# Optimization experiments

Measured on AMD Instinct MI355X. Metric: run time of the kernel, lower is better.

## Reference

```python
import jax, jax.numpy as jnp
import numpy as np

D_MODEL = 1024
NUM_EXPERTS = 64
TOP_K = 2
TEMPERATURE = 1.0


def setup_inputs() -> dict:
    key = jax.random.key(0)
    k1, k2, k3, k4 = jax.random.split(key, 4)
    mh_output = jax.random.normal(k1, (8, 4096, D_MODEL), dtype=jnp.float32)
    noise = jax.random.normal(k2, (8, 4096, NUM_EXPERTS), dtype=jnp.float32)  # randn_like sample, externalized
    # nn.Linear weights: shape [out, in], init normal(0, 0.02); biases zero
    W_route = jax.random.normal(k3, (NUM_EXPERTS, D_MODEL), dtype=jnp.float32) * 0.02
    b_route = jnp.zeros((NUM_EXPERTS,), dtype=jnp.float32)
    W_noise = jax.random.normal(k4, (NUM_EXPERTS, D_MODEL), dtype=jnp.float32) * 0.02
    b_noise = jnp.zeros((NUM_EXPERTS,), dtype=jnp.float32)
    return {"mh_output": mh_output, "noise": noise, "W_route": W_route,
            "b_route": b_route, "W_noise": W_noise, "b_noise": b_noise}


def reference(mh_output, noise, W_route, b_route, W_noise, b_noise):
    # logits = topkroute_linear(mh_output); noise_logits = noise_linear(mh_output)
    logits = jnp.einsum('bsd,ed->bse', mh_output, W_route) + b_route
    noise_logits = jnp.einsum('bsd,ed->bse', mh_output, W_noise) + b_noise
    # noisy logits = logits + temperature * randn * softplus(noise_logits)
    noisy = logits + TEMPERATURE * noise * jax.nn.softplus(noise_logits)
    # top-k, scatter into -inf, softmax  ==  softmax over top-k values scattered into zeros
    top_vals, indices = jax.lax.top_k(noisy, TOP_K)          # [b, s, k]
    probs_k = jax.nn.softmax(top_vals, axis=-1)              # softmax(-inf elsewhere) -> 0 elsewhere
    one_hot = jax.nn.one_hot(indices, NUM_EXPERTS, dtype=noisy.dtype)  # [b, s, k, E]
    router_output = jnp.sum(one_hot * probs_k[..., None], axis=-2)     # [b, s, E]
    return router_output, indices
```

## Files before the change

kernel.cpp:

```cpp
#include <hip/hip_runtime.h>
#include <hip/hip_bf16.h>
#include <math.h>


#define T_TOKENS 32768
#define D_MODEL  1024
#define NE       64
#define NCOL     128
#define M_TILE   32
#define NCHUNK   32
#define CS_LD    68
#define OUT_IDX_BASE ((size_t)T_TOKENS * NE)
#define W_ELEMS  (NCOL * D_MODEL)

typedef short  bf16x8  __attribute__((ext_vector_type(8)));
typedef float  floatx4 __attribute__((ext_vector_type(4)));

__device__ __forceinline__ float softplus_f(float x) {
    return fmaxf(x, 0.f) + log1pf(expf(-fabsf(x)));
}

__device__ __forceinline__ void cvt8(const float4 a, const float4 b,
                                     int4* hi, int4* lo) {
    float v[8] = {a.x, a.y, a.z, a.w, b.x, b.y, b.z, b.w};
    int hw[4], lw[4];
    #pragma unroll
    for (int p = 0; p < 4; ++p) {
        float2 f2 = make_float2(v[2 * p], v[2 * p + 1]);
        __hip_bfloat162 h2 = __float22bfloat162_rn(f2);
        int u; __builtin_memcpy(&u, &h2, 4);
        float h0 = __uint_as_float(((unsigned)u) << 16);
        float h1 = __uint_as_float(((unsigned)u) & 0xFFFF0000u);
        float2 l2 = make_float2(v[2 * p] - h0, v[2 * p + 1] - h1);
        __hip_bfloat162 L2 = __float22bfloat162_rn(l2);
        int ul; __builtin_memcpy(&ul, &L2, 4);
        hw[p] = u; lw[p] = ul;
    }
    *hi = make_int4(hw[0], hw[1], hw[2], hw[3]);
    *lo = make_int4(lw[0], lw[1], lw[2], lw[3]);
}

__device__ __forceinline__ void cvt8r(const float4 a, const float4 b,
                                      bf16x8* hi, bf16x8* lo) {
    int4 h, l;
    cvt8(a, b, &h, &l);
    __builtin_memcpy(hi, &h, 16);
    __builtin_memcpy(lo, &l, 16);
}

__global__ __launch_bounds__(256) void prepack_w(
    const float* __restrict__ Wr, const float* __restrict__ Wn,
    short* __restrict__ Bh, short* __restrict__ Bl)
{
    int g   = blockIdx.x * 256 + threadIdx.x;
    int n   = g & 15;
    int kg  = (g >> 4) & 127;
    int t2  = g >> 11;
    int col = t2 * 16 + n;
    const float* src = (col < NE ? Wr + (size_t)col * D_MODEL
                                 : Wn + (size_t)(col - NE) * D_MODEL) + kg * 8;
    float4 a = *(const float4*)src;
    float4 b = *(const float4*)(src + 4);
    int4 hi, lo;
    cvt8(a, b, &hi, &lo);
    *(int4*)(Bh + (size_t)g * 8) = hi;
    *(int4*)(Bl + (size_t)g * 8) = lo;
}

__global__ __launch_bounds__(256, 4) void router_mfma(
    const float* __restrict__ A,
    const float* __restrict__ noise,
    const float* __restrict__ br,
    const float* __restrict__ bn,
    const short* __restrict__ Bh,
    const short* __restrict__ Bl,
    float* __restrict__ out)
{
    __shared__ float Cs[M_TILE * CS_LD];
    __shared__ float s_p1[M_TILE], s_p2[M_TILE];
    __shared__ int   s_e1[M_TILE], s_e2[M_TILE];

    const int tid  = threadIdx.x;
    const int lane = tid & 63;
    const int wid  = tid >> 6;
    const int n16  = lane & 15;
    const int quad = lane >> 4;
    const int m0   = blockIdx.x * M_TILE;

    const float* pA0 = A + (size_t)(m0 + n16) * D_MODEL + quad * 8;
    const float* pA1 = pA0 + (size_t)16 * D_MODEL;

    const short* pBhR = Bh + ((size_t)(wid * 128 + quad) * 16 + n16) * 8;
    const short* pBlR = Bl + ((size_t)(wid * 128 + quad) * 16 + n16) * 8;
    const short* pBhN = Bh + ((size_t)((4 + wid) * 128 + quad) * 16 + n16) * 8;
    const short* pBlN = Bl + ((size_t)((4 + wid) * 128 + quad) * 16 + n16) * 8;

    floatx4 acc[2][2];
    #pragma unroll
    for (int i = 0; i < 2; ++i) { acc[i][0] = (floatx4)0.f; acc[i][1] = (floatx4)0.f; }

    float4 c0a = *(const float4*)(pA0);
    float4 c0b = *(const float4*)(pA0 + 4);
    float4 c1a = *(const float4*)(pA1);
    float4 c1b = *(const float4*)(pA1 + 4);
    float4 n0a = *(const float4*)(pA0 + 32);
    float4 n0b = *(const float4*)(pA0 + 36);
    float4 n1a = *(const float4*)(pA1 + 32);
    float4 n1b = *(const float4*)(pA1 + 36);

    for (int kc = 0; kc < NCHUNK; ++kc) {
        float4 t0a, t0b, t1a, t1b;
        if (kc + 2 < NCHUNK) {
            const float* q0 = pA0 + (kc + 2) * 32;
            const float* q1 = pA1 + (kc + 2) * 32;
            t0a = *(const float4*)(q0);
            t0b = *(const float4*)(q0 + 4);
            t1a = *(const float4*)(q1);
            t1b = *(const float4*)(q1 + 4);
        }

        const int o = kc * 512;
        bf16x8 bhR = *(const bf16x8*)(pBhR + o);
        bf16x8 blR = *(const bf16x8*)(pBlR + o);
        bf16x8 bhN = *(const bf16x8*)(pBhN + o);
        bf16x8 blN = *(const bf16x8*)(pBlN + o);

        bf16x8 ah0, al0, ah1, al1;
        cvt8r(c0a, c0b, &ah0, &al0);
        cvt8r(c1a, c1b, &ah1, &al1);

        acc[0][0] = __builtin_amdgcn_mfma_f32_16x16x32_bf16(ah0, bhR, acc[0][0], 0, 0, 0);
        acc[0][0] = __builtin_amdgcn_mfma_f32_16x16x32_bf16(ah0, blR, acc[0][0], 0, 0, 0);
        acc[0][0] = __builtin_amdgcn_mfma_f32_16x16x32_bf16(al0, bhR, acc[0][0], 0, 0, 0);
        acc[0][1] = __builtin_amdgcn_mfma_f32_16x16x32_bf16(ah0, bhN, acc[0][1], 0, 0, 0);
        acc[0][1] = __builtin_amdgcn_mfma_f32_16x16x32_bf16(ah0, blN, acc[0][1], 0, 0, 0);
        acc[0][1] = __builtin_amdgcn_mfma_f32_16x16x32_bf16(al0, bhN, acc[0][1], 0, 0, 0);
        acc[1][0] = __builtin_amdgcn_mfma_f32_16x16x32_bf16(ah1, bhR, acc[1][0], 0, 0, 0);
        acc[1][0] = __builtin_amdgcn_mfma_f32_16x16x32_bf16(ah1, blR, acc[1][0], 0, 0, 0);
        acc[1][0] = __builtin_amdgcn_mfma_f32_16x16x32_bf16(al1, bhR, acc[1][0], 0, 0, 0);
        acc[1][1] = __builtin_amdgcn_mfma_f32_16x16x32_bf16(ah1, bhN, acc[1][1], 0, 0, 0);
        acc[1][1] = __builtin_amdgcn_mfma_f32_16x16x32_bf16(ah1, blN, acc[1][1], 0, 0, 0);
        acc[1][1] = __builtin_amdgcn_mfma_f32_16x16x32_bf16(al1, bhN, acc[1][1], 0, 0, 0);

        c0a = n0a; c0b = n0b; c1a = n1a; c1b = n1b;
        n0a = t0a; n0b = t0b; n1a = t1a; n1b = t1b;
    }

    {
        int e = wid * 16 + n16;
        float brv = br[e], bnv = bn[e];
        #pragma unroll
        for (int mf = 0; mf < 2; ++mf)
            #pragma unroll
            for (int rr = 0; rr < 4; ++rr) {
                int t = mf * 16 + quad * 4 + rr;
                float nz    = noise[(size_t)(m0 + t) * NE + e];
                float route = acc[mf][0][rr] + brv;
                float nl    = acc[mf][1][rr] + bnv;
                Cs[t * CS_LD + e] = fmaf(nz, softplus_f(nl), route);
            }
    }
    __syncthreads();

    if (tid < M_TILE) {
        const int t = tid;
        float v1 = -INFINITY, v2 = -INFINITY;
        int e1 = 0, e2 = 0;
        #pragma unroll
        for (int e4 = 0; e4 < 16; ++e4) {
            float4 q = *(const float4*)&Cs[t * CS_LD + e4 * 4];
            float qa[4] = {q.x, q.y, q.z, q.w};
            #pragma unroll
            for (int c = 0; c < 4; ++c) {
                float v = qa[c];
                int e = e4 * 4 + c;
                if (v > v1) { v2 = v1; e2 = e1; v1 = v; e1 = e; }
                else if (v > v2) { v2 = v; e2 = e; }
            }
        }
        float ex = expf(v2 - v1);
        float denom = 1.f + ex;
        s_p1[t] = 1.f / denom;
        s_p2[t] = ex / denom;
        s_e1[t] = e1;
        s_e2[t] = e2;
        float2 iv = make_float2((float)e1, (float)e2);
        *(float2*)(out + OUT_IDX_BASE + (size_t)(m0 + t) * 2) = iv;
    }
    __syncthreads();

    #pragma unroll
    for (int i = 0; i < 2; ++i) {
        int gi = i * 256 + tid;
        int t  = gi >> 4;
        int e0 = (gi & 15) * 4;
        float p1 = s_p1[t], p2 = s_p2[t];
        int   e1 = s_e1[t], e2 = s_e2[t];
        float4 v;
        v.x = (e0 + 0 == e1) ? p1 : ((e0 + 0 == e2) ? p2 : 0.f);
        v.y = (e0 + 1 == e1) ? p1 : ((e0 + 1 == e2) ? p2 : 0.f);
        v.z = (e0 + 2 == e1) ? p1 : ((e0 + 2 == e2) ? p2 : 0.f);
        v.w = (e0 + 3 == e1) ? p1 : ((e0 + 3 == e2) ? p2 : 0.f);
        *(float4*)(out + (size_t)(m0 + t) * NE + e0) = v;
    }
}

extern "C" void kernel_launch(void* const* d_in, const int* in_sizes, int n_in,
                              void* d_out, int out_size, void* d_ws, size_t ws_size,
                              hipStream_t stream) {
    const float* A     = (const float*)d_in[0];
    const float* noise = (const float*)d_in[1];
    const float* Wr    = (const float*)d_in[2];
    const float* br    = (const float*)d_in[3];
    const float* Wn    = (const float*)d_in[4];
    const float* bn    = (const float*)d_in[5];
    float* out = (float*)d_out;

    short* Bh = (short*)d_ws;
    short* Bl = Bh + W_ELEMS;

    prepack_w<<<dim3(W_ELEMS / 8 / 256), dim3(256), 0, stream>>>(Wr, Wn, Bh, Bl);
    router_mfma<<<dim3(T_TOKENS / M_TILE), dim3(256), 0, stream>>>(A, noise, br, bn, Bh, Bl, out);
}
```

Baseline: 261.3 us.

## Stream activation tiles via global_load_lds ring buffer with doubled token tile

Replaces per-thread register prefetch of the fp32 activations with asynchronous global-to-LDS loads into a 4-deep swizzled ring buffer, synchronized with explicit vmcnt waits and barriers. The token tile doubles from 32 to 64, so each weight fragment load is reused across four MFMA row groups, and weight fragments are now prefetched one chunk ahead. The aim is to hide memory latency and halve weight traffic per token. In exchange, occupancy drops from 4 to 2 blocks per SM, LDS use rises, and every chunk now needs a block-wide barrier.

Measured after the change: 236.8 us. 1.1x faster.

```diff
diff --git a/kernel.cpp b/kernel.cpp
--- a/kernel.cpp
+++ b/kernel.cpp
@@ -7,14 +7,17 @@
 #define D_MODEL  1024
 #define NE       64
 #define NCOL     128
-#define M_TILE   32
+#define M_TILE   64
 #define NCHUNK   32
+#define RING_D   4
 #define CS_LD    68
 #define OUT_IDX_BASE ((size_t)T_TOKENS * NE)
 #define W_ELEMS  (NCOL * D_MODEL)
 
 typedef short  bf16x8  __attribute__((ext_vector_type(8)));
 typedef float  floatx4 __attribute__((ext_vector_type(4)));
+typedef const __attribute__((address_space(1))) unsigned int gu32;
+typedef __attribute__((address_space(3))) unsigned int lu32;
 
 __device__ __forceinline__ float softplus_f(float x) {
     return fmaxf(x, 0.f) + log1pf(expf(-fabsf(x)));
@@ -67,7 +70,7 @@
     *(int4*)(Bl + (size_t)g * 8) = lo;
 }
 
-__global__ __launch_bounds__(256, 4) void router_mfma(
+__global__ __launch_bounds__(256, 2) void router_mfma(
     const float* __restrict__ A,
     const float* __restrict__ noise,
     const float* __restrict__ br,
@@ -76,6 +79,7 @@
     const short* __restrict__ Bl,
     float* __restrict__ out)
 {
+    __shared__ __align__(16) float ringA[RING_D * M_TILE * 32];
     __shared__ float Cs[M_TILE * CS_LD];
     __shared__ float s_p1[M_TILE], s_p2[M_TILE];
     __shared__ int   s_e1[M_TILE], s_e2[M_TILE];
@@ -87,70 +91,89 @@
     const int quad = lane >> 4;
     const int m0   = blockIdx.x * M_TILE;
 
-    const float* pA0 = A + (size_t)(m0 + n16) * D_MODEL + quad * 8;
-    const float* pA1 = pA0 + (size_t)16 * D_MODEL;
+    const int rlo = lane >> 3;
+    const int csw = ((lane & 7) ^ rlo) * 4;
+    const int j0  = 2 * wid;
+    const float* srcA0 = A + (size_t)(m0 + j0 * 8 + rlo) * D_MODEL + csw;
+    const float* srcA1 = A + (size_t)(m0 + j0 * 8 + 8 + rlo) * D_MODEL + csw;
+
+    const int sw0 = (((quad * 32 +  0) ^ ((n16 & 7) << 4)) >> 2);
+    const int sw1 = (((quad * 32 + 16) ^ ((n16 & 7) << 4)) >> 2);
 
     const short* pBhR = Bh + ((size_t)(wid * 128 + quad) * 16 + n16) * 8;
     const short* pBlR = Bl + ((size_t)(wid * 128 + quad) * 16 + n16) * 8;
     const short* pBhN = Bh + ((size_t)((4 + wid) * 128 + quad) * 16 + n16) * 8;
     const short* pBlN = Bl + ((size_t)((4 + wid) * 128 + quad) * 16 + n16) * 8;
 
-    floatx4 acc[2][2];
+#define DMA_CHUNK(KC_) do {                                                   \
+        const int b_ = (KC_) & (RING_D - 1);                                  \
+        __builtin_amdgcn_global_load_lds(                                     \
+            (gu32*)(srcA0 + (KC_) * 32),                                      \
+            (lu32*)(ringA + b_ * (M_TILE * 32) + j0 * 256), 16, 0, 0);        \
+        __builtin_amdgcn_global_load_lds(                                     \
+            (gu32*)(srcA1 + (KC_) * 32),                                      \
+            (lu32*)(ringA + b_ * (M_TILE * 32) + (j0 + 1) * 256), 16, 0, 0);  \
+    } while (0)
+
+    floatx4 acc[4][2];
     #pragma unroll
-    for (int i = 0; i < 2; ++i) { acc[i][0] = (floatx4)0.f; acc[i][1] = (floatx4)0.f; }
-
-    float4 c0a = *(const float4*)(pA0);
-    float4 c0b = *(const float4*)(pA0 + 4);
-    float4 c1a = *(const float4*)(pA1);
-    float4 c1b = *(const float4*)(pA1 + 4);
-    float4 n0a = *(const float4*)(pA0 + 32);
-    float4 n0b = *(const float4*)(pA0 + 36);
-    float4 n1a = *(const float4*)(pA1 + 32);
-    float4 n1b = *(const float4*)(pA1 + 36);
+    for (int i = 0; i < 4; ++i) { acc[i][0] = (floatx4)0.f; acc[i][1] = (floatx4)0.f; }
+
+    DMA_CHUNK(0);
+    DMA_CHUNK(1);
+    DMA_CHUNK(2);
+    bf16x8 bhR = *(const bf16x8*)(pBhR);
+    bf16x8 blR = *(const bf16x8*)(pBlR);
+    bf16x8 bhN = *(const bf16x8*)(pBhN);
+    bf16x8 blN = *(const bf16x8*)(pBlN);
 
     for (int kc = 0; kc < NCHUNK; ++kc) {
-        float4 t0a, t0b, t1a, t1b;
-        if (kc + 2 < NCHUNK) {
-            const float* q0 = pA0 + (kc + 2) * 32;
-            const float* q1 = pA1 + (kc + 2) * 32;
-            t0a = *(const float4*)(q0);
-            t0b = *(const float4*)(q0 + 4);
-            t1a = *(const float4*)(q1);
-            t1b = *(const float4*)(q1 + 4);
+        const int buf = kc & (RING_D - 1);
+
+        __builtin_amdgcn_sched_barrier(0);
+        if (kc < NCHUNK - 2)       asm volatile("s_waitcnt vmcnt(4)" ::: "memory");
+        else if (kc == NCHUNK - 2) asm volatile("s_waitcnt vmcnt(2)" ::: "memory");
+        else                       asm volatile("s_waitcnt vmcnt(0)" ::: "memory");
+        __builtin_amdgcn_s_barrier();
+        __builtin_amdgcn_sched_barrier(0);
+
+        if (kc + RING_D - 1 < NCHUNK) DMA_CHUNK(kc + RING_D - 1);
+
+        const int on = (kc + 1 < NCHUNK ? kc + 1 : kc) * 512;
+        bf16x8 nbhR = *(const bf16x8*)(pBhR + on);
+        bf16x8 nblR = *(const bf16x8*)(pBlR + on);
+        bf16x8 nbhN = *(const bf16x8*)(pBhN + on);
+        bf16x8 nblN = *(const bf16x8*)(pBlN + on);
+
+        float4 fa[4], fb[4];
+        #pragma unroll
+        for (int mf = 0; mf < 4; ++mf) {
+            const float* p = &ringA[buf * (M_TILE * 32) + (mf * 16 + n16) * 32];
+            fa[mf] = *(const float4*)(p + sw0);
+            fb[mf] = *(const float4*)(p + sw1);
         }
 
-        const int o = kc * 512;
-        bf16x8 bhR = *(const bf16x8*)(pBhR + o);
-        bf16x8 blR = *(const bf16x8*)(pBlR + o);
-        bf16x8 bhN = *(const bf16x8*)(pBhN + o);
-        bf16x8 blN = *(const bf16x8*)(pBlN + o);
-
-        bf16x8 ah0, al0, ah1, al1;
-        cvt8r(c0a, c0b, &ah0, &al0);
-        cvt8r(c1a, c1b, &ah1, &al1);
-
-        acc[0][0] = __builtin_amdgcn_mfma_f32_16x16x32_bf16(ah0, bhR, acc[0][0], 0, 0, 0);
-        acc[0][0] = __builtin_amdgcn_mfma_f32_16x16x32_bf16(ah0, blR, acc[0][0], 0, 0, 0);
-        acc[0][0] = __builtin_amdgcn_mfma_f32_16x16x32_bf16(al0, bhR, acc[0][0], 0, 0, 0);
-        acc[0][1] = __builtin_amdgcn_mfma_f32_16x16x32_bf16(ah0, bhN, acc[0][1], 0, 0, 0);
-        acc[0][1] = __builtin_amdgcn_mfma_f32_16x16x32_bf16(ah0, blN, acc[0][1], 0, 0, 0);
-        acc[0][1] = __builtin_amdgcn_mfma_f32_16x16x32_bf16(al0, bhN, acc[0][1], 0, 0, 0);
-        acc[1][0] = __builtin_amdgcn_mfma_f32_16x16x32_bf16(ah1, bhR, acc[1][0], 0, 0, 0);
-        acc[1][0] = __builtin_amdgcn_mfma_f32_16x16x32_bf16(ah1, blR, acc[1][0], 0, 0, 0);
-        acc[1][0] = __builtin_amdgcn_mfma_f32_16x16x32_bf16(al1, bhR, acc[1][0], 0, 0, 0);
-        acc[1][1] = __builtin_amdgcn_mfma_f32_16x16x32_bf16(ah1, bhN, acc[1][1], 0, 0, 0);
-        acc[1][1] = __builtin_amdgcn_mfma_f32_16x16x32_bf16(ah1, blN, acc[1][1], 0, 0, 0);
-        acc[1][1] = __builtin_amdgcn_mfma_f32_16x16x32_bf16(al1, bhN, acc[1][1], 0, 0, 0);
-
-        c0a = n0a; c0b = n0b; c1a = n1a; c1b = n1b;
-        n0a = t0a; n0b = t0b; n1a = t1a; n1b = t1b;
-    }
+        #pragma unroll
+        for (int mf = 0; mf < 4; ++mf) {
+            bf16x8 ah, al;
+            cvt8r(fa[mf], fb[mf], &ah, &al);
+            acc[mf][0] = __builtin_amdgcn_mfma_f32_16x16x32_bf16(ah, bhR, acc[mf][0], 0, 0, 0);
+            acc[mf][0] = __builtin_amdgcn_mfma_f32_16x16x32_bf16(ah, blR, acc[mf][0], 0, 0, 0);
+            acc[mf][0] = __builtin_amdgcn_mfma_f32_16x16x32_bf16(al, bhR, acc[mf][0], 0, 0, 0);
+            acc[mf][1] = __builtin_amdgcn_mfma_f32_16x16x32_bf16(ah, bhN, acc[mf][1], 0, 0, 0);
+            acc[mf][1] = __builtin_amdgcn_mfma_f32_16x16x32_bf16(ah, blN, acc[mf][1], 0, 0, 0);
+            acc[mf][1] = __builtin_amdgcn_mfma_f32_16x16x32_bf16(al, bhN, acc[mf][1], 0, 0, 0);
+        }
+
+        bhR = nbhR; blR = nblR; bhN = nbhN; blN = nblN;
+    }
+#undef DMA_CHUNK
 
     {
         int e = wid * 16 + n16;
         float brv = br[e], bnv = bn[e];
         #pragma unroll
-        for (int mf = 0; mf < 2; ++mf)
+        for (int mf = 0; mf < 4; ++mf)
             #pragma unroll
             for (int rr = 0; rr < 4; ++rr) {
                 int t = mf * 16 + quad * 4 + rr;
@@ -190,7 +213,7 @@
     __syncthreads();
 
     #pragma unroll
-    for (int i = 0; i < 2; ++i) {
+    for (int i = 0; i < 4; ++i) {
         int gi = i * 256 + tid;
         int t  = gi >> 4;
         int e0 = (gi & 15) * 4;
```
